# Kernel tuning notes

Measured on AMD Instinct MI355X. Metric: run time of the kernel, lower is better.

The kernel has to match this reference:

```python
import jax, jax.numpy as jnp
import numpy as np

B, S, F, RANK = 8, 4096, 1024, 64


def gram_schmidt(P):
    """Sequential Gram-Schmidt on columns of P (F, R) -> orthogonal (unnormalized) columns.
    Matches vizbert's orth_tensor: v_i = p_i - sum_{j<i} ((u_j . v)/(u_j . u_j)) u_j.
    Each step vectorizes the inner projection loop as one matmul (u_j are mutually
    orthogonal, so sequential-update and batched coefficients are equal in exact math)."""
    us = [P[:, 0]]
    for i in range(1, P.shape[1]):
        U = jnp.stack(us, axis=1)                 # (F, i)
        sq = jnp.sum(U * U, axis=0)               # (i,)
        v = P[:, i]
        coeff = (U.T @ v) / sq                    # (i,)
        us.append(v - U @ coeff)
    return jnp.stack(us, axis=1)                  # (F, R)


def setup_inputs() -> dict:
    key = jax.random.key(0)
    k1, k2 = jax.random.split(key)
    hidden_states = jax.random.normal(k1, (B, S, F), dtype=jnp.float32)
    # probe params initialized uniform(-0.05, 0.05), stacked to (num_features, rank)
    probe = jax.random.uniform(k2, (F, RANK), minval=-0.05, maxval=0.05, dtype=jnp.float32)
    return {"hidden_states": hidden_states, "probe": probe}


def reference(hidden_states, probe):
    # orth_probe: Gram-Schmidt orthogonalized probe columns (orthogonalize=True)
    U = gram_schmidt(probe)                       # (F, R), orthogonal columns
    sq = jnp.sum(U * U, axis=0)                   # (R,) squared norms

    # normalize=True: remember per-token norms before projection
    old_norms = jnp.linalg.norm(hidden_states, axis=2, keepdims=True)  # (B, S, 1)
    # mask_first=True: remember first-token states
    first_state = hidden_states[:, 0]             # (B, F)

    # full_batch_gs: subtract projection onto each probe direction.
    # Because U's columns are orthogonal, the sequential per-column subtraction
    # equals one fused projection: h - U (U^T h / ||u||^2).
    coeffs = jnp.einsum('bsf,fr->bsr', hidden_states, U) / sq
    h = hidden_states - jnp.einsum('bsr,fr->bsf', coeffs, U)

    # normalize=True: rescale back to the original per-token norm
    new_norms = jnp.linalg.norm(h, axis=2, keepdims=True)
    h = h / new_norms * old_norms

    # mask_first=True: restore the first token untouched
    h = h.at[:, 0].set(first_state)
    return h
```

## Files before the change

### kernel.cpp

```cpp
#include <hip/hip_runtime.h>
#include <hip/hip_bf16.h>


typedef __attribute__((ext_vector_type(8))) short bf16x8;
typedef __attribute__((ext_vector_type(4))) float f32x4;

#define MFMA_B16(a, b, c) __builtin_amdgcn_mfma_f32_16x16x32_bf16((a), (b), (c), 0, 0, 0)

__device__ __forceinline__ unsigned short bf16bits(float x) {
  union { float f; unsigned u; } v; v.f = x;
  return (unsigned short)((v.u + 0x7fffu + ((v.u >> 16) & 1u)) >> 16);
}

__device__ __forceinline__ bf16x8 packbf8(f32x4 v0, f32x4 v1) {
  union { bf16x8 v; __hip_bfloat162 h[4]; } u;
  u.h[0] = __float22bfloat162_rn(make_float2(v0[0], v0[1]));
  u.h[1] = __float22bfloat162_rn(make_float2(v0[2], v0[3]));
  u.h[2] = __float22bfloat162_rn(make_float2(v1[0], v1[1]));
  u.h[3] = __float22bfloat162_rn(make_float2(v1[2], v1[3]));
  return u.v;
}

__device__ __forceinline__ bf16x8 cvt8(const float* p) {
  return packbf8(*(const f32x4*)p, *(const f32x4*)(p + 4));
}

__global__ void pp_prep(const float* __restrict__ P, float* __restrict__ partial,
                        unsigned short* __restrict__ Ptb, unsigned short* __restrict__ Pb) {
  __shared__ float Pl[64][68];
  const int tid = threadIdx.x, ch = blockIdx.x;
  #pragma unroll
  for (int u = 0; u < 4; ++u) {
    const int f = tid >> 2, r = (tid & 3) * 16 + 4 * u;
    *(f32x4*)&Pl[f][r] = *(const f32x4*)(P + (size_t)(ch * 64 + f) * 64 + r);
  }
  __syncthreads();
  const int a0 = (tid >> 4) * 4, b0 = (tid & 15) * 4;
  f32x4 acc[4];
  #pragma unroll
  for (int i = 0; i < 4; ++i) acc[i] = (f32x4){0.f, 0.f, 0.f, 0.f};
  for (int k = 0; k < 64; ++k) {
    f32x4 av = *(const f32x4*)&Pl[k][a0];
    f32x4 bv = *(const f32x4*)&Pl[k][b0];
    #pragma unroll
    for (int i = 0; i < 4; ++i) acc[i] += av[i] * bv;
  }
  #pragma unroll
  for (int i = 0; i < 4; ++i)
    *(f32x4*)(partial + (size_t)ch * 4096 + (size_t)(a0 + i) * 64 + b0) = acc[i];
  const int f = tid >> 2, c0 = (tid & 3) * 16;
  const int gf = ch * 64 + f;
  unsigned short b16[16];
  #pragma unroll
  for (int u = 0; u < 16; ++u) b16[u] = bf16bits(Pl[f][c0 + u]);
  #pragma unroll
  for (int u = 0; u < 16; ++u) Ptb[(size_t)(c0 + u) * 1024 + gf] = b16[u];
  #pragma unroll
  for (int w = 0; w < 4; ++w) {
    unsigned long long q = (unsigned long long)b16[4 * w] |
                           ((unsigned long long)b16[4 * w + 1] << 16) |
                           ((unsigned long long)b16[4 * w + 2] << 32) |
                           ((unsigned long long)b16[4 * w + 3] << 48);
    *(unsigned long long*)(Pb + (size_t)gf * 64 + c0 + 4 * w) = q;
  }
}

__global__ void pp_invert(const float* __restrict__ partial, unsigned short* __restrict__ Wb) {
  __shared__ float A[64][68];
  const int tid = threadIdx.x;
  const int i = tid >> 2, q16 = (tid & 3) * 16;
  #pragma unroll
  for (int u = 0; u < 4; ++u) {
    f32x4 s = (f32x4){0.f, 0.f, 0.f, 0.f};
    const int off = i * 64 + q16 + 4 * u;
    for (int p = 0; p < 16; ++p) s += *(const f32x4*)(partial + (size_t)p * 4096 + off);
    *(f32x4*)&A[i][q16 + 4 * u] = s;
  }
  __syncthreads();
  for (int k = 0; k < 64; ++k) {
    const float d = 1.0f / A[k][k];
    const float f = A[i][k];
    f32x4 prs[4], cur[4];
    #pragma unroll
    for (int u = 0; u < 4; ++u) {
      prs[u] = *(const f32x4*)&A[k][q16 + 4 * u];
      cur[u] = *(const f32x4*)&A[i][q16 + 4 * u];
    }
    __syncthreads();
    const int kl = k - q16;
    #pragma unroll
    for (int u = 0; u < 4; ++u) {
      f32x4 pv = prs[u] * d;
      if (kl >= u * 4 && kl < u * 4 + 4) { pv[kl - u * 4] = d; cur[u][kl - u * 4] = 0.f; }
      f32x4 res = (i == k) ? pv : (cur[u] - f * pv);
      *(f32x4*)&A[i][q16 + 4 * u] = res;
    }
    __syncthreads();
  }
  #pragma unroll
  for (int u = 0; u < 4; ++u) {
    #pragma unroll
    for (int j = 0; j < 4; ++j) Wb[(size_t)i * 64 + q16 + 4 * u + j] = bf16bits(A[i][q16 + 4 * u + j]);
  }
}

__global__ __launch_bounds__(256, 4) void pp_main(
    const float* __restrict__ H, const unsigned short* __restrict__ Ptb,
    const unsigned short* __restrict__ Pb, const unsigned short* __restrict__ Wb,
    float* __restrict__ out) {
  __shared__ float Yl[4][16][68];
  __shared__ float Cl[4][16][68];

  const int tid = threadIdx.x, wid = tid >> 6, lane = tid & 63;
  const int c16 = lane & 15, quad = lane >> 4;
  const long rowbase = (long)blockIdx.x * 64 + wid * 16;
  const float* hrow = H + (rowbase + c16) * 1024 + quad * 8;

  f32x4 accY[4];
  #pragma unroll
  for (int t = 0; t < 4; ++t) accY[t] = (f32x4){0.f, 0.f, 0.f, 0.f};
  float sq = 0.f;
  const unsigned short* pB = Ptb + (size_t)c16 * 1024 + quad * 8;
  #pragma unroll 4
  for (int kk = 0; kk < 32; ++kk) {
    f32x4 v0 = *(const f32x4*)(hrow + kk * 32);
    f32x4 v1 = *(const f32x4*)(hrow + kk * 32 + 4);
    sq += v0[0] * v0[0] + v0[1] * v0[1] + v0[2] * v0[2] + v0[3] * v0[3];
    sq += v1[0] * v1[0] + v1[1] * v1[1] + v1[2] * v1[2] + v1[3] * v1[3];
    bf16x8 a = packbf8(v0, v1);
    #pragma unroll
    for (int t = 0; t < 4; ++t) {
      bf16x8 b = *(const bf16x8*)(pB + (size_t)t * 16 * 1024 + kk * 32);
      accY[t] = MFMA_B16(a, b, accY[t]);
    }
  }
  sq += __shfl_xor(sq, 16, 64);
  sq += __shfl_xor(sq, 32, 64);
  #pragma unroll
  for (int t = 0; t < 4; ++t)
    #pragma unroll
    for (int r = 0; r < 4; ++r)
      Yl[wid][quad * 4 + r][t * 16 + c16] = accY[t][r];
  __syncthreads();

  bf16x8 ya0 = cvt8(&Yl[wid][c16][quad * 8]);
  bf16x8 ya1 = cvt8(&Yl[wid][c16][32 + quad * 8]);
  f32x4 accC[4];
  #pragma unroll
  for (int t = 0; t < 4; ++t) accC[t] = (f32x4){0.f, 0.f, 0.f, 0.f};
  const unsigned short* wB = Wb + (size_t)c16 * 64 + quad * 8;
  #pragma unroll
  for (int t = 0; t < 4; ++t) {
    bf16x8 b0 = *(const bf16x8*)(wB + (size_t)t * 16 * 64);
    bf16x8 b1 = *(const bf16x8*)(wB + (size_t)t * 16 * 64 + 32);
    accC[t] = MFMA_B16(ya0, b0, accC[t]);
    accC[t] = MFMA_B16(ya1, b1, accC[t]);
  }
  #pragma unroll
  for (int t = 0; t < 4; ++t)
    #pragma unroll
    for (int r = 0; r < 4; ++r) Cl[wid][quad * 4 + r][t * 16 + c16] = accC[t][r];
  __syncthreads();

  float d = 0.f;
  #pragma unroll
  for (int u = 0; u < 4; ++u) {
    f32x4 yv = *(const f32x4*)&Yl[wid][c16][quad * 16 + 4 * u];
    f32x4 cv = *(const f32x4*)&Cl[wid][c16][quad * 16 + 4 * u];
    d += yv[0] * cv[0] + yv[1] * cv[1] + yv[2] * cv[2] + yv[3] * cv[3];
  }
  d += __shfl_xor(d, 16, 64);
  d += __shfl_xor(d, 32, 64);
  const float scl = sqrtf(sq / fmaxf(sq - d, 1e-30f));

  bf16x8 ca0 = cvt8(&Cl[wid][c16][quad * 8]);
  bf16x8 ca1 = cvt8(&Cl[wid][c16][32 + quad * 8]);
  float sc[4]; long rg[4]; bool fs[4];
  #pragma unroll
  for (int r = 0; r < 4; ++r) {
    const int m = quad * 4 + r;
    sc[r] = __shfl(scl, m, 64);
    rg[r] = rowbase + m;
    fs[r] = ((rg[r] & 4095) == 0);
  }
  const unsigned short* pb3 = Pb + (size_t)c16 * 64 + quad * 8;
  #pragma unroll 2
  for (int ft = 0; ft < 64; ++ft) {
    bf16x8 b0 = *(const bf16x8*)(pb3 + (size_t)ft * 16 * 64);
    bf16x8 b1 = *(const bf16x8*)(pb3 + (size_t)ft * 16 * 64 + 32);
    f32x4 acc = (f32x4){0.f, 0.f, 0.f, 0.f};
    acc = MFMA_B16(ca0, b0, acc);
    acc = MFMA_B16(ca1, b1, acc);
    const int f = ft * 16 + c16;
    #pragma unroll
    for (int r = 0; r < 4; ++r) {
      const long idx = rg[r] * 1024 + f;
      const float h = H[idx];
      const float o = fs[r] ? h : (h - acc[r]) * sc[r];
      __builtin_nontemporal_store(o, &out[idx]);
    }
  }
}

extern "C" void kernel_launch(void* const* d_in, const int* in_sizes, int n_in,
                              void* d_out, int out_size, void* d_ws, size_t ws_size,
                              hipStream_t stream) {
  const float* H = (const float*)d_in[0];
  const float* P = (const float*)d_in[1];
  float* out = (float*)d_out;
  float* ws = (float*)d_ws;
  float* partial = ws;
  unsigned short* Ptb = (unsigned short*)(ws + 16 * 4096);
  unsigned short* Pb = Ptb + 65536;
  unsigned short* Wb = Pb + 65536;

  pp_prep<<<16, 256, 0, stream>>>(P, partial, Ptb, Pb);
  pp_invert<<<1, 256, 0, stream>>>(partial, Wb);
  pp_main<<<512, 256, 0, stream>>>(H, Ptb, Pb, Wb, out);
}
```

Baseline: 328.5 us.

## Split each block's rows across warps by feature chunks with LDS reduction

```diff
diff --git a/kernel.cpp b/kernel.cpp
--- a/kernel.cpp
+++ b/kernel.cpp
@@ -24,6 +24,9 @@
 __device__ __forceinline__ bf16x8 cvt8(const float* p) {
   return packbf8(*(const f32x4*)p, *(const f32x4*)(p + 4));
 }
+__device__ __forceinline__ float dot4(f32x4 a, f32x4 b) {
+  return a[0] * b[0] + a[1] * b[1] + a[2] * b[2] + a[3] * b[3];
+}
 
 __global__ void pp_prep(const float* __restrict__ P, float* __restrict__ partial,
                         unsigned short* __restrict__ Ptb, unsigned short* __restrict__ Pb) {
@@ -104,29 +107,32 @@
   }
 }
 
-__global__ __launch_bounds__(256, 4) void pp_main(
+__global__ __launch_bounds__(256, 7) void pp_main(
     const float* __restrict__ H, const unsigned short* __restrict__ Ptb,
     const unsigned short* __restrict__ Pb, const unsigned short* __restrict__ Wb,
     float* __restrict__ out) {
-  __shared__ float Yl[4][16][68];
-  __shared__ float Cl[4][16][68];
+  __shared__ float Yp[4][16][68];
+  __shared__ float Cl[16][68];
+  __shared__ float rowsq[16];
 
   const int tid = threadIdx.x, wid = tid >> 6, lane = tid & 63;
   const int c16 = lane & 15, quad = lane >> 4;
-  const long rowbase = (long)blockIdx.x * 64 + wid * 16;
-  const float* hrow = H + (rowbase + c16) * 1024 + quad * 8;
-
+  const unsigned row0 = (unsigned)blockIdx.x * 16;
+
+  if (tid < 16) rowsq[tid] = 0.f;
+  __syncthreads();
+
+  const float* hrow = H + (size_t)(row0 + c16) * 1024 + wid * 256 + quad * 8;
+  const unsigned short* pB = Ptb + (size_t)c16 * 1024 + wid * 256 + quad * 8;
   f32x4 accY[4];
   #pragma unroll
   for (int t = 0; t < 4; ++t) accY[t] = (f32x4){0.f, 0.f, 0.f, 0.f};
   float sq = 0.f;
-  const unsigned short* pB = Ptb + (size_t)c16 * 1024 + quad * 8;
-  #pragma unroll 4
-  for (int kk = 0; kk < 32; ++kk) {
+  #pragma unroll
+  for (int kk = 0; kk < 8; ++kk) {
     f32x4 v0 = *(const f32x4*)(hrow + kk * 32);
     f32x4 v1 = *(const f32x4*)(hrow + kk * 32 + 4);
-    sq += v0[0] * v0[0] + v0[1] * v0[1] + v0[2] * v0[2] + v0[3] * v0[3];
-    sq += v1[0] * v1[0] + v1[1] * v1[1] + v1[2] * v1[2] + v1[3] * v1[3];
+    sq += dot4(v0, v0) + dot4(v1, v1);
     bf16x8 a = packbf8(v0, v1);
     #pragma unroll
     for (int t = 0; t < 4; ++t) {
@@ -136,65 +142,64 @@
   }
   sq += __shfl_xor(sq, 16, 64);
   sq += __shfl_xor(sq, 32, 64);
+  if (lane < 16) atomicAdd(&rowsq[c16], sq);
   #pragma unroll
   for (int t = 0; t < 4; ++t)
     #pragma unroll
     for (int r = 0; r < 4; ++r)
-      Yl[wid][quad * 4 + r][t * 16 + c16] = accY[t][r];
-  __syncthreads();
-
-  bf16x8 ya0 = cvt8(&Yl[wid][c16][quad * 8]);
-  bf16x8 ya1 = cvt8(&Yl[wid][c16][32 + quad * 8]);
-  f32x4 accC[4];
-  #pragma unroll
-  for (int t = 0; t < 4; ++t) accC[t] = (f32x4){0.f, 0.f, 0.f, 0.f};
-  const unsigned short* wB = Wb + (size_t)c16 * 64 + quad * 8;
-  #pragma unroll
-  for (int t = 0; t < 4; ++t) {
-    bf16x8 b0 = *(const bf16x8*)(wB + (size_t)t * 16 * 64);
-    bf16x8 b1 = *(const bf16x8*)(wB + (size_t)t * 16 * 64 + 32);
-    accC[t] = MFMA_B16(ya0, b0, accC[t]);
-    accC[t] = MFMA_B16(ya1, b1, accC[t]);
-  }
-  #pragma unroll
-  for (int t = 0; t < 4; ++t)
-    #pragma unroll
-    for (int r = 0; r < 4; ++r) Cl[wid][quad * 4 + r][t * 16 + c16] = accC[t][r];
-  __syncthreads();
-
-  float d = 0.f;
-  #pragma unroll
-  for (int u = 0; u < 4; ++u) {
-    f32x4 yv = *(const f32x4*)&Yl[wid][c16][quad * 16 + 4 * u];
-    f32x4 cv = *(const f32x4*)&Cl[wid][c16][quad * 16 + 4 * u];
-    d += yv[0] * cv[0] + yv[1] * cv[1] + yv[2] * cv[2] + yv[3] * cv[3];
-  }
+      Yp[wid][quad * 4 + r][t * 16 + c16] = accY[t][r];
+  __syncthreads();
+
+  f32x4 ys0a = {0.f,0.f,0.f,0.f}, ys0b = {0.f,0.f,0.f,0.f};
+  f32x4 ys1a = {0.f,0.f,0.f,0.f}, ys1b = {0.f,0.f,0.f,0.f};
+  #pragma unroll
+  for (int w2 = 0; w2 < 4; ++w2) {
+    ys0a += *(const f32x4*)&Yp[w2][c16][quad * 8];
+    ys0b += *(const f32x4*)&Yp[w2][c16][quad * 8 + 4];
+    ys1a += *(const f32x4*)&Yp[w2][c16][32 + quad * 8];
+    ys1b += *(const f32x4*)&Yp[w2][c16][32 + quad * 8 + 4];
+  }
+  bf16x8 ya0 = packbf8(ys0a, ys0b);
+  bf16x8 ya1 = packbf8(ys1a, ys1b);
+  const unsigned short* wB = Wb + (size_t)(wid * 16 + c16) * 64 + quad * 8;
+  f32x4 accC = (f32x4){0.f, 0.f, 0.f, 0.f};
+  accC = MFMA_B16(ya0, *(const bf16x8*)wB, accC);
+  accC = MFMA_B16(ya1, *(const bf16x8*)(wB + 32), accC);
+  #pragma unroll
+  for (int r = 0; r < 4; ++r) Cl[quad * 4 + r][wid * 16 + c16] = accC[r];
+  const float o2 = rowsq[c16];
+  __syncthreads();
+
+  float d = dot4(ys0a, *(const f32x4*)&Cl[c16][quad * 8]) +
+            dot4(ys0b, *(const f32x4*)&Cl[c16][quad * 8 + 4]) +
+            dot4(ys1a, *(const f32x4*)&Cl[c16][32 + quad * 8]) +
+            dot4(ys1b, *(const f32x4*)&Cl[c16][32 + quad * 8 + 4]);
   d += __shfl_xor(d, 16, 64);
   d += __shfl_xor(d, 32, 64);
-  const float scl = sqrtf(sq / fmaxf(sq - d, 1e-30f));
-
-  bf16x8 ca0 = cvt8(&Cl[wid][c16][quad * 8]);
-  bf16x8 ca1 = cvt8(&Cl[wid][c16][32 + quad * 8]);
-  float sc[4]; long rg[4]; bool fs[4];
+  const float scl = sqrtf(o2 / fmaxf(o2 - d, 1e-30f));
+
+  bf16x8 ca0 = cvt8(&Cl[c16][quad * 8]);
+  bf16x8 ca1 = cvt8(&Cl[c16][32 + quad * 8]);
+  float sc[4]; unsigned rg[4]; bool fs[4];
   #pragma unroll
   for (int r = 0; r < 4; ++r) {
     const int m = quad * 4 + r;
     sc[r] = __shfl(scl, m, 64);
-    rg[r] = rowbase + m;
-    fs[r] = ((rg[r] & 4095) == 0);
-  }
-  const unsigned short* pb3 = Pb + (size_t)c16 * 64 + quad * 8;
-  #pragma unroll 2
-  for (int ft = 0; ft < 64; ++ft) {
+    rg[r] = row0 + m;
+    fs[r] = ((rg[r] & 4095u) == 0u);
+  }
+  const unsigned short* pb3 = Pb + ((size_t)wid * 16 * 16 + c16) * 64 + quad * 8;
+  #pragma unroll 4
+  for (int ft = 0; ft < 16; ++ft) {
     bf16x8 b0 = *(const bf16x8*)(pb3 + (size_t)ft * 16 * 64);
     bf16x8 b1 = *(const bf16x8*)(pb3 + (size_t)ft * 16 * 64 + 32);
     f32x4 acc = (f32x4){0.f, 0.f, 0.f, 0.f};
     acc = MFMA_B16(ca0, b0, acc);
     acc = MFMA_B16(ca1, b1, acc);
-    const int f = ft * 16 + c16;
+    const unsigned f = (unsigned)(wid * 16 + ft) * 16 + c16;
     #pragma unroll
     for (int r = 0; r < 4; ++r) {
-      const long idx = rg[r] * 1024 + f;
+      const size_t idx = (size_t)rg[r] * 1024 + f;
       const float h = H[idx];
       const float o = fs[r] ? h : (h - acc[r]) * sc[r];
       __builtin_nontemporal_store(o, &out[idx]);
@@ -216,5 +221,5 @@
 
   pp_prep<<<16, 256, 0, stream>>>(P, partial, Ptb, Pb);
   pp_invert<<<1, 256, 0, stream>>>(partial, Wb);
-  pp_main<<<512, 256, 0, stream>>>(H, Ptb, Pb, Wb, out);
-}
+  pp_main<<<2048, 256, 0, stream>>>(H, Ptb, Pb, Wb, out);
+}
```

Result: slower. 354.6 us (+8.0%).
